# Performance work log

Measured on AMD Instinct MI355X. Metric: run time of the kernel, lower is better.

The kernel has to match this reference:

```python
import jax, jax.numpy as jnp
import numpy as np

HIDDEN = 2048
HEADS = 16
HEAD_DIM = HIDDEN // HEADS
BLOCK = 64
SEQ = 4096
NUM_BLOCKS = SEQ // BLOCK
N_LOCAL = 3
N_GLOBAL = 1
N_RANDOM = 1
SCALE = 1.0 / np.sqrt(HEAD_DIM)


def _sparse_mask(rand_idx):
    # rand_idx: [num_blocks, n_random] int -- random key-block per query-block row
    i = jnp.arange(NUM_BLOCKS)[:, None]
    j = jnp.arange(NUM_BLOCKS)[None, :]
    half = N_LOCAL // 2
    local = (j >= i - half) & (j <= i + half)
    glob = (j < N_GLOBAL) | (j >= NUM_BLOCKS - N_GLOBAL)
    rand = jnp.any(j[:, :, None] == rand_idx[:, None, :], axis=-1)
    blk = local | glob | rand                      # [nb, nb] bool
    full = jnp.repeat(jnp.repeat(blk, BLOCK, axis=0), BLOCK, axis=1)
    return full[:SEQ, :SEQ]                        # [S, S] bool


def setup_inputs() -> dict:
    key = jax.random.key(0)
    k1, k2, k3, k4, k5, k6 = jax.random.split(key, 6)
    s = 0.02
    return {
        "hidden_states": jax.random.normal(k1, (1, SEQ, HIDDEN), jnp.float32),
        "rand_idx": jax.random.randint(k2, (NUM_BLOCKS, N_RANDOM), 0, NUM_BLOCKS, jnp.int32),
        "Wq": jax.random.normal(k3, (HIDDEN, HIDDEN), jnp.float32) * s,
        "Wk": jax.random.normal(k4, (HIDDEN, HIDDEN), jnp.float32) * s,
        "Wv": jax.random.normal(k5, (HIDDEN, HIDDEN), jnp.float32) * s,
        "Wo": jax.random.normal(k6, (HIDDEN, HIDDEN), jnp.float32) * s,
    }


def reference(hidden_states, rand_idx, Wq, Wk, Wv, Wo):
    B, S, _ = hidden_states.shape
    # torch Linear: y = x @ W.T
    q = (hidden_states @ Wq.T).reshape(B, S, HEADS, HEAD_DIM).transpose(0, 2, 1, 3)
    k = (hidden_states @ Wk.T).reshape(B, S, HEADS, HEAD_DIM).transpose(0, 2, 1, 3)
    v = (hidden_states @ Wv.T).reshape(B, S, HEADS, HEAD_DIM).transpose(0, 2, 1, 3)
    scores = jnp.einsum("bhqd,bhkd->bhqk", q, k) * SCALE
    mask = _sparse_mask(rand_idx)                  # [S, S] bool
    scores = jnp.where(mask[None, None, :, :], scores, -jnp.inf)
    probs = jax.nn.softmax(scores, axis=-1)
    out = jnp.einsum("bhqk,bhkd->bhqd", probs, v)
    out = out.transpose(0, 2, 1, 3).reshape(B, S, HIDDEN)
    return out @ Wo.T
```

## Files before the change

### kernel.cpp

```cpp
#include <hip/hip_runtime.h>

typedef unsigned short u16;
typedef __bf16 bf16x8 __attribute__((ext_vector_type(8)));
typedef float f32x4 __attribute__((ext_vector_type(4)));

#define SEQQ 4096
#define HID 2048
#define HD 128
#define NBLK 64
#define ATT_SCALE 0.08838834764831843f

__device__ __forceinline__ u16 f2bf(float f) {
    unsigned u = __float_as_uint(f);
    u += 0x7fffu + ((u >> 16) & 1u);
    return (u16)(u >> 16);
}

__device__ __forceinline__ void gload_lds16(const void* g, void* l) {
    __builtin_amdgcn_global_load_lds((const __attribute__((address_space(1))) void*)g,
                                     (__attribute__((address_space(3))) void*)l, 16, 0, 0);
}

__global__ __launch_bounds__(256) void cvt_bf16_k(const float* __restrict__ in,
                                                  u16* __restrict__ out, int n4) {
    int i = blockIdx.x * 256 + threadIdx.x;
    if (i < n4) {
        float4 v = ((const float4*)in)[i];
        ushort4 o;
        o.x = f2bf(v.x); o.y = f2bf(v.y); o.z = f2bf(v.z); o.w = f2bf(v.w);
        ((ushort4*)out)[i] = o;
    }
}

template <int MODE>
__global__ __launch_bounds__(256) void gemm_bt(const u16* __restrict__ A,
                                               const u16* __restrict__ B,
                                               void* __restrict__ C,
                                               int M, int N, int K) {
    __shared__ __align__(16) u16 As[128 * 32];
    __shared__ __align__(16) u16 Bs[128 * 32];
    const int t = threadIdx.x, w = t >> 6, l = t & 63;
    const int lg = l >> 4, ll = l & 15;
    const int mb = blockIdx.y, nb = blockIdx.x;
    const int wr = w >> 1, wc = w & 1;

    f32x4 acc[4][4] = {};

    const int sr = l >> 2;
    const int sc = (l & 3) * 8;
    const u16* gA = A + (mb * 128 + w * 16 + sr) * K + sc;
    const u16* gB = B + (nb * 128 + w * 16 + sr) * K + sc;
    char* lA0 = (char*)As + w * 1024;
    char* lA1 = (char*)As + (w + 4) * 1024;
    char* lB0 = (char*)Bs + w * 1024;
    char* lB1 = (char*)Bs + (w + 4) * 1024;

    for (int kt = 0; kt < K; kt += 32) {
        __syncthreads();
        gload_lds16(gA + kt, lA0);
        gload_lds16(gA + 64 * K + kt, lA1);
        gload_lds16(gB + kt, lB0);
        gload_lds16(gB + 64 * K + kt, lB1);
        __syncthreads();

        bf16x8 af[4], bfr[4];
#pragma unroll
        for (int mi = 0; mi < 4; ++mi)
            af[mi] = *(const bf16x8*)&As[(wr * 64 + mi * 16 + ll) * 32 + lg * 8];
#pragma unroll
        for (int ni = 0; ni < 4; ++ni)
            bfr[ni] = *(const bf16x8*)&Bs[(wc * 64 + ni * 16 + ll) * 32 + lg * 8];
#pragma unroll
        for (int mi = 0; mi < 4; ++mi)
#pragma unroll
            for (int ni = 0; ni < 4; ++ni)
                acc[mi][ni] = __builtin_amdgcn_mfma_f32_16x16x32_bf16(af[mi], bfr[ni],
                                                                      acc[mi][ni], 0, 0, 0);
    }

    const int row0 = mb * 128 + wr * 64, col0 = nb * 128 + wc * 64;
#pragma unroll
    for (int mi = 0; mi < 4; ++mi)
#pragma unroll
        for (int ni = 0; ni < 4; ++ni) {
            f32x4 v = acc[mi][ni];
#pragma unroll
            for (int r = 0; r < 4; ++r) {
                int row = row0 + mi * 16 + lg * 4 + r;
                int col = col0 + ni * 16 + ll;
                if (MODE == 0)
                    ((float*)C)[row * N + col] = v[r];
                else if (MODE == 1)
                    ((u16*)C)[row * N + col] = f2bf(v[r]);
                else
                    ((u16*)C)[col * M + row] = f2bf(v[r]);
            }
        }
}

__global__ __launch_bounds__(256) void sparse_attn(const u16* __restrict__ Q,
                                                   const u16* __restrict__ Kmat,
                                                   const u16* __restrict__ Vt,
                                                   const int* __restrict__ rnd,
                                                   u16* __restrict__ Out) {
    __shared__ __align__(16) char Plds[4 * 2048];
    const int qb = blockIdx.x, h = blockIdx.y;
    const int t = threadIdx.x, w = t >> 6, l = t & 63;
    const int lg = l >> 4, ll = l & 15;

    int blist[6];
    int nblk = 0;
    {
        int cands[6];
        cands[0] = qb - 1; cands[1] = qb; cands[2] = qb + 1;
        cands[3] = 0; cands[4] = NBLK - 1; cands[5] = rnd[qb];
        for (int c = 0; c < 6; ++c) {
            int b = cands[c];
            if (b < 0 || b >= NBLK) continue;
            bool dup = false;
            for (int j = 0; j < nblk; ++j) dup = dup || (blist[j] == b);
            if (!dup) blist[nblk++] = b;
        }
    }

    bf16x8 qf[4];
    const int qrow = qb * 64 + w * 16 + ll;
#pragma unroll
    for (int kc = 0; kc < 4; ++kc)
        qf[kc] = *(const bf16x8*)&Q[qrow * HID + h * HD + kc * 32 + lg * 8];

    f32x4 o[8];
#pragma unroll
    for (int dt = 0; dt < 8; ++dt) o[dt] = (f32x4){0.f, 0.f, 0.f, 0.f};
    float mrun[4], lrun[4];
#pragma unroll
    for (int r = 0; r < 4; ++r) { mrun[r] = -1e30f; lrun[r] = 0.f; }

    char* Pw = Plds + w * 2048;

    for (int bi = 0; bi < nblk; ++bi) {
        const int kb = blist[bi];

        f32x4 s[4];
#pragma unroll
        for (int ct = 0; ct < 4; ++ct) s[ct] = (f32x4){0.f, 0.f, 0.f, 0.f};
#pragma unroll
        for (int ct = 0; ct < 4; ++ct) {
#pragma unroll
            for (int kc = 0; kc < 4; ++kc) {
                bf16x8 kf = *(const bf16x8*)&Kmat[(kb * 64 + ct * 16 + ll) * HID +
                                                  h * HD + kc * 32 + lg * 8];
                s[ct] = __builtin_amdgcn_mfma_f32_16x16x32_bf16(qf[kc], kf, s[ct], 0, 0, 0);
            }
        }

        float rmax[4];
#pragma unroll
        for (int r = 0; r < 4; ++r) {
            s[0][r] *= ATT_SCALE; s[1][r] *= ATT_SCALE;
            s[2][r] *= ATT_SCALE; s[3][r] *= ATT_SCALE;
            rmax[r] = fmaxf(fmaxf(s[0][r], s[1][r]), fmaxf(s[2][r], s[3][r]));
        }
#pragma unroll
        for (int mk = 1; mk <= 8; mk <<= 1)
#pragma unroll
            for (int r = 0; r < 4; ++r)
                rmax[r] = fmaxf(rmax[r], __shfl_xor(rmax[r], mk));

        float scl[4], psum[4];
#pragma unroll
        for (int r = 0; r < 4; ++r) {
            float mn = fmaxf(mrun[r], rmax[r]);
            scl[r] = __expf(mrun[r] - mn);
            mrun[r] = mn;
            psum[r] = 0.f;
        }

#pragma unroll
        for (int ct = 0; ct < 4; ++ct)
#pragma unroll
            for (int r = 0; r < 4; ++r) {
                float e = __expf(s[ct][r] - mrun[r]);
                psum[r] += e;
                const int q = lg * 4 + r;
                const int kv = ct * 16 + ll;
                *(u16*)(Pw + q * 128 + ((kv * 2) ^ ((q & 7) << 4))) = f2bf(e);
            }
#pragma unroll
        for (int mk = 1; mk <= 8; mk <<= 1)
#pragma unroll
            for (int r = 0; r < 4; ++r)
                psum[r] += __shfl_xor(psum[r], mk);
#pragma unroll
        for (int r = 0; r < 4; ++r)
            lrun[r] = lrun[r] * scl[r] + psum[r];
#pragma unroll
        for (int dt = 0; dt < 8; ++dt)
#pragma unroll
            for (int r = 0; r < 4; ++r)
                o[dt][r] *= scl[r];

#pragma unroll
        for (int kc2 = 0; kc2 < 2; ++kc2) {
            bf16x8 pf = *(const bf16x8*)(Pw + ll * 128 +
                                         ((kc2 * 64 + lg * 16) ^ ((ll & 7) << 4)));
#pragma unroll
            for (int dt = 0; dt < 8; ++dt) {
                bf16x8 vf = *(const bf16x8*)&Vt[(h * HD + dt * 16 + ll) * SEQQ +
                                                kb * 64 + kc2 * 32 + lg * 8];
                o[dt] = __builtin_amdgcn_mfma_f32_16x16x32_bf16(pf, vf, o[dt], 0, 0, 0);
            }
        }
    }

    float rl[4];
#pragma unroll
    for (int r = 0; r < 4; ++r) rl[r] = 1.f / lrun[r];
#pragma unroll
    for (int dt = 0; dt < 8; ++dt)
#pragma unroll
        for (int r = 0; r < 4; ++r) {
            int row = qb * 64 + w * 16 + lg * 4 + r;
            int col = h * HD + dt * 16 + ll;
            Out[row * HID + col] = f2bf(o[dt][r] * rl[r]);
        }
}

extern "C" void kernel_launch(void* const* d_in, const int* in_sizes, int n_in,
                              void* d_out, int out_size, void* d_ws, size_t ws_size,
                              hipStream_t stream) {
    const float* hs = (const float*)d_in[0];
    const int* rnd = (const int*)d_in[1];
    const float* Wq = (const float*)d_in[2];
    const float* Wk = (const float*)d_in[3];
    const float* Wv = (const float*)d_in[4];
    const float* Wo = (const float*)d_in[5];
    float* out = (float*)d_out;

    char* ws = (char*)d_ws;
    u16* hs_b = (u16*)(ws);
    u16* Wq_b = (u16*)(ws + 16777216);
    u16* Wk_b = (u16*)(ws + 25165824);
    u16* Wv_b = (u16*)(ws + 33554432);
    u16* Wo_b = (u16*)(ws + 41943040);
    u16* Qb   = (u16*)(ws + 50331648);
    u16* Kb   = (u16*)(ws + 67108864);
    u16* Vtb  = (u16*)(ws + 83886080);
    u16* Ab   = (u16*)(ws + 100663296);

    cvt_bf16_k<<<dim3(8192), 256, 0, stream>>>(hs, hs_b, 8388608 / 4);
    cvt_bf16_k<<<dim3(4096), 256, 0, stream>>>(Wq, Wq_b, 4194304 / 4);
    cvt_bf16_k<<<dim3(4096), 256, 0, stream>>>(Wk, Wk_b, 4194304 / 4);
    cvt_bf16_k<<<dim3(4096), 256, 0, stream>>>(Wv, Wv_b, 4194304 / 4);
    cvt_bf16_k<<<dim3(4096), 256, 0, stream>>>(Wo, Wo_b, 4194304 / 4);

    dim3 gg(2048 / 128, 4096 / 128);
    gemm_bt<1><<<gg, 256, 0, stream>>>(hs_b, Wq_b, Qb, 4096, 2048, 2048);
    gemm_bt<1><<<gg, 256, 0, stream>>>(hs_b, Wk_b, Kb, 4096, 2048, 2048);
    gemm_bt<2><<<gg, 256, 0, stream>>>(hs_b, Wv_b, Vtb, 4096, 2048, 2048);

    sparse_attn<<<dim3(64, 16), 256, 0, stream>>>(Qb, Kb, Vtb, rnd, Ab);

    gemm_bt<0><<<gg, 256, 0, stream>>>(Ab, Wo_b, out, 4096, 2048, 2048);
}
```

Measured before the change: 476.4 us.

## Fuse QKV projections, batch weight conversion, swizzle GEMM grid, LDS double-buffer attention

```diff
diff --git a/kernel.cpp b/kernel.cpp
--- a/kernel.cpp
+++ b/kernel.cpp
@@ -32,6 +32,22 @@
     }
 }
 
+__global__ __launch_bounds__(256) void cvt4_k(const float* __restrict__ w0,
+                                              const float* __restrict__ w1,
+                                              const float* __restrict__ w2,
+                                              const float* __restrict__ w3,
+                                              u16* __restrict__ qkv,
+                                              u16* __restrict__ wo) {
+    const int y = blockIdx.y;
+    const float* src = (y == 0) ? w0 : (y == 1) ? w1 : (y == 2) ? w2 : w3;
+    u16* dst = (y < 3) ? (qkv + (size_t)y * 4194304) : wo;
+    int i = blockIdx.x * 256 + threadIdx.x;
+    float4 v = ((const float4*)src)[i];
+    ushort4 o;
+    o.x = f2bf(v.x); o.y = f2bf(v.y); o.z = f2bf(v.z); o.w = f2bf(v.w);
+    ((ushort4*)dst)[i] = o;
+}
+
 template <int MODE>
 __global__ __launch_bounds__(256) void gemm_bt(const u16* __restrict__ A,
                                                const u16* __restrict__ B,
@@ -41,15 +57,22 @@
     __shared__ __align__(16) u16 Bs[128 * 32];
     const int t = threadIdx.x, w = t >> 6, l = t & 63;
     const int lg = l >> 4, ll = l & 15;
-    const int mb = blockIdx.y, nb = blockIdx.x;
+
+    const int gx = gridDim.x, gy = gridDim.y;
+    const int nwg = gx * gy;
+    int lid = blockIdx.y * gx + blockIdx.x;
+    int swz = (lid & 7) * (nwg >> 3) + (lid >> 3);
+    const int mb = swz % gy;
+    const int nb = swz / gy;
+
     const int wr = w >> 1, wc = w & 1;
 
     f32x4 acc[4][4] = {};
 
     const int sr = l >> 2;
     const int sc = (l & 3) * 8;
-    const u16* gA = A + (mb * 128 + w * 16 + sr) * K + sc;
-    const u16* gB = B + (nb * 128 + w * 16 + sr) * K + sc;
+    const u16* gA = A + (size_t)(mb * 128 + w * 16 + sr) * K + sc;
+    const u16* gB = B + (size_t)(nb * 128 + w * 16 + sr) * K + sc;
     char* lA0 = (char*)As + w * 1024;
     char* lA1 = (char*)As + (w + 4) * 1024;
     char* lB0 = (char*)Bs + w * 1024;
@@ -58,9 +81,9 @@
     for (int kt = 0; kt < K; kt += 32) {
         __syncthreads();
         gload_lds16(gA + kt, lA0);
-        gload_lds16(gA + 64 * K + kt, lA1);
+        gload_lds16(gA + (size_t)64 * K + kt, lA1);
         gload_lds16(gB + kt, lB0);
-        gload_lds16(gB + 64 * K + kt, lB1);
+        gload_lds16(gB + (size_t)64 * K + kt, lB1);
         __syncthreads();
 
         bf16x8 af[4], bfr[4];
@@ -88,12 +111,17 @@
             for (int r = 0; r < 4; ++r) {
                 int row = row0 + mi * 16 + lg * 4 + r;
                 int col = col0 + ni * 16 + ll;
-                if (MODE == 0)
-                    ((float*)C)[row * N + col] = v[r];
-                else if (MODE == 1)
-                    ((u16*)C)[row * N + col] = f2bf(v[r]);
-                else
-                    ((u16*)C)[col * M + row] = f2bf(v[r]);
+                if (MODE == 0) {
+                    ((float*)C)[(size_t)row * N + col] = v[r];
+                } else {
+                    u16* Cq = (u16*)C;
+                    if (col < 2048)
+                        Cq[(size_t)row * 2048 + col] = f2bf(v[r]);
+                    else if (col < 4096)
+                        Cq[8388608 + (size_t)row * 2048 + (col - 2048)] = f2bf(v[r]);
+                    else
+                        Cq[16777216 + (size_t)(col - 4096) * 4096 + row] = f2bf(v[r]);
+                }
             }
         }
 }
@@ -103,7 +131,10 @@
                                                    const u16* __restrict__ Vt,
                                                    const int* __restrict__ rnd,
                                                    u16* __restrict__ Out) {
+    __shared__ __align__(16) u16 Ks[2][8192];
+    __shared__ __align__(16) u16 Vs[2][8192];
     __shared__ __align__(16) char Plds[4 * 2048];
+
     const int qb = blockIdx.x, h = blockIdx.y;
     const int t = threadIdx.x, w = t >> 6, l = t & 63;
     const int lg = l >> 4, ll = l & 15;
@@ -123,11 +154,24 @@
         }
     }
 
+    auto stage = [&](int buf, int kb) {
+        const u16* kbase = Kmat + (size_t)(kb * 64) * HID + h * HD;
+        const u16* vbase = Vt + (size_t)(h * HD) * SEQQ + kb * 64;
+#pragma unroll
+        for (int j = 0; j < 4; ++j) {
+            int d = j * 256 + t;
+            int kr = d >> 4, kc_ = (d & 15) ^ (kr & 7);
+            gload_lds16(kbase + (size_t)kr * HID + kc_ * 8, &Ks[buf][d * 8]);
+            int vr = d >> 3, vc = (d & 7) ^ (vr & 7);
+            gload_lds16(vbase + (size_t)vr * SEQQ + vc * 8, &Vs[buf][d * 8]);
+        }
+    };
+
     bf16x8 qf[4];
     const int qrow = qb * 64 + w * 16 + ll;
 #pragma unroll
     for (int kc = 0; kc < 4; ++kc)
-        qf[kc] = *(const bf16x8*)&Q[qrow * HID + h * HD + kc * 32 + lg * 8];
+        qf[kc] = *(const bf16x8*)&Q[(size_t)qrow * HID + h * HD + kc * 32 + lg * 8];
 
     f32x4 o[8];
 #pragma unroll
@@ -138,18 +182,27 @@
 
     char* Pw = Plds + w * 2048;
 
+    stage(0, blist[0]);
+    int cur = 0;
+
     for (int bi = 0; bi < nblk; ++bi) {
-        const int kb = blist[bi];
+        if (bi + 1 < nblk) {
+            stage(cur ^ 1, blist[bi + 1]);
+            asm volatile("s_waitcnt vmcnt(8)\n\ts_barrier" ::: "memory");
+        } else {
+            asm volatile("s_waitcnt vmcnt(0)\n\ts_barrier" ::: "memory");
+        }
 
         f32x4 s[4];
 #pragma unroll
         for (int ct = 0; ct < 4; ++ct) s[ct] = (f32x4){0.f, 0.f, 0.f, 0.f};
 #pragma unroll
         for (int ct = 0; ct < 4; ++ct) {
+            const int krow = ct * 16 + ll;
 #pragma unroll
             for (int kc = 0; kc < 4; ++kc) {
-                bf16x8 kf = *(const bf16x8*)&Kmat[(kb * 64 + ct * 16 + ll) * HID +
-                                                  h * HD + kc * 32 + lg * 8];
+                bf16x8 kf = *(const bf16x8*)&Ks[cur][krow * 128 +
+                                                    (((kc * 4 + lg) ^ (krow & 7)) << 3)];
                 s[ct] = __builtin_amdgcn_mfma_f32_16x16x32_bf16(qf[kc], kf, s[ct], 0, 0, 0);
             }
         }
@@ -206,11 +259,15 @@
                                          ((kc2 * 64 + lg * 16) ^ ((ll & 7) << 4)));
 #pragma unroll
             for (int dt = 0; dt < 8; ++dt) {
-                bf16x8 vf = *(const bf16x8*)&Vt[(h * HD + dt * 16 + ll) * SEQQ +
-                                                kb * 64 + kc2 * 32 + lg * 8];
+                const int vrow = dt * 16 + ll;
+                bf16x8 vf = *(const bf16x8*)&Vs[cur][vrow * 64 +
+                                                     (((kc2 * 4 + lg) ^ (vrow & 7)) << 3)];
                 o[dt] = __builtin_amdgcn_mfma_f32_16x16x32_bf16(pf, vf, o[dt], 0, 0, 0);
             }
         }
+
+        asm volatile("s_barrier" ::: "memory");
+        cur ^= 1;
     }
 
     float rl[4];
@@ -222,7 +279,7 @@
         for (int r = 0; r < 4; ++r) {
             int row = qb * 64 + w * 16 + lg * 4 + r;
             int col = h * HD + dt * 16 + ll;
-            Out[row * HID + col] = f2bf(o[dt][r] * rl[r]);
+            Out[(size_t)row * HID + col] = f2bf(o[dt][r] * rl[r]);
         }
 }
 
@@ -238,28 +295,20 @@
     float* out = (float*)d_out;
 
     char* ws = (char*)d_ws;
-    u16* hs_b = (u16*)(ws);
-    u16* Wq_b = (u16*)(ws + 16777216);
-    u16* Wk_b = (u16*)(ws + 25165824);
-    u16* Wv_b = (u16*)(ws + 33554432);
-    u16* Wo_b = (u16*)(ws + 41943040);
-    u16* Qb   = (u16*)(ws + 50331648);
-    u16* Kb   = (u16*)(ws + 67108864);
-    u16* Vtb  = (u16*)(ws + 83886080);
-    u16* Ab   = (u16*)(ws + 100663296);
+    u16* hs_b   = (u16*)(ws);
+    u16* Wqkv_b = (u16*)(ws + 16777216);
+    u16* Wo_b   = (u16*)(ws + 41943040);
+    u16* Qb     = (u16*)(ws + 50331648);
+    u16* Kb     = (u16*)(ws + 67108864);
+    u16* Vtb    = (u16*)(ws + 83886080);
+    u16* Ab     = (u16*)(ws + 100663296);
 
     cvt_bf16_k<<<dim3(8192), 256, 0, stream>>>(hs, hs_b, 8388608 / 4);
-    cvt_bf16_k<<<dim3(4096), 256, 0, stream>>>(Wq, Wq_b, 4194304 / 4);
-    cvt_bf16_k<<<dim3(4096), 256, 0, stream>>>(Wk, Wk_b, 4194304 / 4);
-    cvt_bf16_k<<<dim3(4096), 256, 0, stream>>>(Wv, Wv_b, 4194304 / 4);
-    cvt_bf16_k<<<dim3(4096), 256, 0, stream>>>(Wo, Wo_b, 4194304 / 4);
-
-    dim3 gg(2048 / 128, 4096 / 128);
-    gemm_bt<1><<<gg, 256, 0, stream>>>(hs_b, Wq_b, Qb, 4096, 2048, 2048);
-    gemm_bt<1><<<gg, 256, 0, stream>>>(hs_b, Wk_b, Kb, 4096, 2048, 2048);
-    gemm_bt<2><<<gg, 256, 0, stream>>>(hs_b, Wv_b, Vtb, 4096, 2048, 2048);
+    cvt4_k<<<dim3(4096, 4), 256, 0, stream>>>(Wq, Wk, Wv, Wo, Wqkv_b, Wo_b);
+
+    gemm_bt<3><<<dim3(48, 32), 256, 0, stream>>>(hs_b, Wqkv_b, Qb, 4096, 6144, 2048);
 
     sparse_attn<<<dim3(64, 16), 256, 0, stream>>>(Qb, Kb, Vtb, rnd, Ab);
 
-    gemm_bt<0><<<gg, 256, 0, stream>>>(Ab, Wo_b, out, 4096, 2048, 2048);
-}
+    gemm_bt<0><<<dim3(16, 32), 256, 0, stream>>>(Ab, Wo_b, out, 4096, 2048, 2048);
+}
```

Result: faster. 417.5 us (-12.4%).
